# Performance work log

Measured on AMD Instinct MI355X. Metric: run time of the kernel, lower is better.

Reference implementation:

```python
import jax, jax.numpy as jnp
import numpy as np

D = 32          # embedding_size
B = 16384       # batch_size
P = 16          # neighbor_sample_size (paths per item per hop)
NE = 100000     # n_entity
NU = 100000     # n_user
NR = 32         # n_relation
N_ITER = 2


def setup_inputs() -> dict:
    key = jax.random.key(0)
    ks = jax.random.split(key, 20)
    s = 0.1
    nrm = lambda k, sh: jax.random.normal(k, sh, dtype=jnp.float32) * s
    inp = {
        "user_table": nrm(ks[0], (NU, D)),
        "ent_table": nrm(ks[1], (NE, D)),
        "rel_table": nrm(ks[2], (NR, D)),
        # PyTorch LSTM params, gate order (i, f, g, o)
        "w_ih0": nrm(ks[3], (4 * D, 2 * D)),
        "w_hh0": nrm(ks[4], (4 * D, D)),
        "b_ih0": nrm(ks[5], (4 * D,)),
        "b_hh0": nrm(ks[6], (4 * D,)),
        "w_ih1": nrm(ks[7], (4 * D, 2 * D)),
        "w_hh1": nrm(ks[8], (4 * D, D)),
        "b_ih1": nrm(ks[9], (4 * D,)),
        "b_hh1": nrm(ks[10], (4 * D,)),
        "agg_w": nrm(ks[11], (D, D)),
        "agg_b": nrm(ks[12], (D,)),
        "users": jax.random.randint(ks[13], (B,), 0, NU),
        "items": jax.random.randint(ks[14], (B,), 0, NE),
        "ratings": jax.random.randint(ks[15], (B,), 0, 2),
        # hop h path table: [n_entity, P, 2*(h+1)+1]; values < 32 valid for both tables
        "lp0": jax.random.randint(ks[16], (NE, P, 3), 0, 32),
        "lp1": jax.random.randint(ks[17], (NE, P, 5), 0, 32),
    }
    return inp


def _lstm_last(seq, w_ih, w_hh, b_ih, b_hh):
    # seq: [N, T, 2D] -> final hidden state [N, D], PyTorch gate order i,f,g,o
    N = seq.shape[0]
    H = w_hh.shape[1]
    bias = b_ih + b_hh

    def step(carry, x):
        h, c = carry
        g = x @ w_ih.T + h @ w_hh.T + bias
        i, f, gg, o = jnp.split(g, 4, axis=-1)
        c = jax.nn.sigmoid(f) * c + jax.nn.sigmoid(i) * jnp.tanh(gg)
        h = jax.nn.sigmoid(o) * jnp.tanh(c)
        return (h, c), None

    h0 = jnp.zeros((N, H), seq.dtype)
    (h, _), _ = jax.lax.scan(step, (h0, h0), jnp.swapaxes(seq, 0, 1))
    return h


def _forward(user_table, ent_table, rel_table, lstm_params, agg_w, agg_b,
             users, items, ratings, lps):
    u = user_table[users]                # [B, D]
    items_emb = ent_table[items]         # [B, D]
    for hop in range(N_ITER):
        lp = lps[hop]
        w_ih, w_hh, b_ih, b_hh = lstm_params[hop]
        il = lp[items]                   # [B, P, 2*(hop+1)+1]
        seed_e = ent_table[il[:, :, 0]]  # [B, P, D]
        u_b = jnp.broadcast_to(u[:, None, :], seed_e.shape)
        first = jnp.concatenate([u_b, seed_e], -1)[:, :, None, :]   # [B,P,1,2D]
        rel_e = rel_table[il[:, :, 1::2]]                            # [B,P,hop+1,D]
        tail_e = ent_table[il[:, :, 2::2]]                           # [B,P,hop+1,D]
        rest = jnp.concatenate([rel_e, tail_e], -1)                  # [B,P,hop+1,2D]
        seq = jnp.concatenate([first, rest], 2).reshape(B * P, hop + 2, 2 * D)
        h = _lstm_last(seq, w_ih, w_hh, b_ih, b_hh)                  # [B*P, D]
        final = h.reshape(B, P, D).sum(axis=1)                       # hidden_out sum
        items_emb = (items_emb + final) @ agg_w.T + agg_b            # 'sum' aggregator
    scores = jnp.sum(u * items_emb, axis=-1)                         # [B]
    r = ratings.astype(scores.dtype)
    # stable BCE on sigmoid(scores)
    loss = -jnp.mean(r * jax.nn.log_sigmoid(scores) + (1.0 - r) * jax.nn.log_sigmoid(-scores))
    return loss, jax.nn.sigmoid(scores)


def reference(user_table, ent_table, rel_table,
              w_ih0, w_hh0, b_ih0, b_hh0,
              w_ih1, w_hh1, b_ih1, b_hh1,
              agg_w, agg_b,
              users, items, ratings, lp0, lp1):
    lstm_params = [(w_ih0, w_hh0, b_ih0, b_hh0), (w_ih1, w_hh1, b_ih1, b_hh1)]
    loss, scores_normalized = _forward(user_table, ent_table, rel_table,
                                       lstm_params, agg_w, agg_b,
                                       users, items, ratings, (lp0, lp1))
    return (loss, scores_normalized, items)
```

## Files before the change

### kernel.cpp

```cpp
#include <hip/hip_runtime.h>
#include <math.h>

#define D  32
#define BN 16384
#define PP 16

typedef __bf16 bf16x8 __attribute__((ext_vector_type(8)));
typedef __bf16 bf16x4 __attribute__((ext_vector_type(4)));
typedef float  floatx4 __attribute__((ext_vector_type(4)));

#define K1 1.44269504088896341f
#define K2 2.88539008177792681f

#define TR_OFF    0
#define TE_OFF    8448
#define BIAS_OFF  16896
#define WU_OFF    17408
#define WHH_OFF   27648
#define IMG_BYTES 37888
#define LDS_BYTES (IMG_BYTES + 8 * 1280)

__device__ __forceinline__ float sigf(float x) {
    float e = __builtin_amdgcn_exp2f(-x * K1);
    return __builtin_amdgcn_rcpf(1.0f + e);
}
__device__ __forceinline__ float logsigf(float x) {
    float ax = fabsf(x);
    float l = log1pf(__expf(-ax));
    return (x >= 0.0f) ? -l : x - l;
}
__device__ __forceinline__ floatx4 cvt4(bf16x4 v) {
    floatx4 r = { (float)v[0], (float)v[1], (float)v[2], (float)v[3] };
    return r;
}
__device__ __forceinline__ bf16x8 loadu8(const float* __restrict__ p) {
    float4 a = ((const float4*)p)[0], b = ((const float4*)p)[1];
    bf16x8 r = { (__bf16)a.x, (__bf16)a.y, (__bf16)a.z, (__bf16)a.w,
                 (__bf16)b.x, (__bf16)b.y, (__bf16)b.z, (__bf16)b.w };
    return r;
}

__global__ __launch_bounds__(256)
void prep_tables(const float* __restrict__ ent, const float* __restrict__ rel,
                 const float* __restrict__ wih0, const float* __restrict__ whh0,
                 const float* __restrict__ bih0, const float* __restrict__ bhh0,
                 const float* __restrict__ wih1, const float* __restrict__ whh1,
                 const float* __restrict__ bih1, const float* __restrict__ bhh1,
                 float* __restrict__ imgs_f)
{
    const int id = blockIdx.x * 256 + threadIdx.x;
    if (id < 16384) {
        const int hop = id >> 13;
        const int rest = id & 8191;
        const int tab = rest >> 12;
        const int k   = (rest >> 7) & 31;
        const int g   = rest & 127;
        const float* wih = hop ? wih1 : wih0;
        char* base = (char*)imgs_f + (size_t)hop * IMG_BYTES;
        if (tab == 0) {
            const float* w = wih + (size_t)g * 64;
            const float* s = rel + (size_t)k * 32;
            float a = (hop ? bih1[g] + bhh1[g] : bih0[g] + bhh0[g]);
            #pragma unroll
            for (int d = 0; d < 32; ++d) a = fmaf(w[d], s[d], a);
            *((__bf16*)(base + TR_OFF) + k * 132 + g) = (__bf16)a;
        } else {
            const float* w = wih + (size_t)g * 64 + 32;
            const float* s = ent + (size_t)k * 32;
            float a = 0.0f;
            #pragma unroll
            for (int d = 0; d < 32; ++d) a = fmaf(w[d], s[d], a);
            *((__bf16*)(base + TE_OFF) + k * 132 + g) = (__bf16)a;
        }
    } else if (id < 32768) {
        const int id2 = id - 16384;
        const int hop = id2 >> 13;
        const int rest = id2 & 8191;
        const int mat  = rest >> 12;
        const int e    = rest & 4095;
        const int gate = e >> 5, d = e & 31;
        char* base = (char*)imgs_f + (size_t)hop * IMG_BYTES;
        float v;
        if (mat == 0) v = (hop ? wih1 : wih0)[(size_t)gate * 64 + d];
        else          v = (hop ? whh1 : whh0)[(size_t)gate * 32 + d];
        *((__bf16*)(base + (mat ? WHH_OFF : WU_OFF)) + gate * 40 + d) = (__bf16)v;
    } else if (id < 33024) {
        const int id3 = id - 32768;
        const int hop = id3 >> 7;
        const int g   = id3 & 127;
        char* base = (char*)imgs_f + (size_t)hop * IMG_BYTES;
        ((float*)(base + BIAS_OFF))[g] = hop ? (bih1[g] + bhh1[g])
                                             : (bih0[g] + bhh0[g]);
    }
}

template<bool FIRST, bool LAST>
__device__ __forceinline__ void nonlin(
    floatx4* __restrict__ acc, float* __restrict__ cst,
    float* __restrict__ hlo, float* __restrict__ hhi,
    char* __restrict__ Hw, int q, int bnl)
{
    #pragma unroll
    for (int hf = 0; hf < 2; ++hf) {
        float* hout = hf ? hhi : hlo;
        #pragma unroll
        for (int r = 0; r < 4; ++r) {
            float gi = acc[0 + hf][r], gf = acc[2 + hf][r],
                  gg = acc[4 + hf][r], go = acc[6 + hf][r];
            float Ai = 1.0f + __builtin_amdgcn_exp2f(-gi * K1);
            float Af = 1.0f + __builtin_amdgcn_exp2f(-gf * K1);
            float G2 = __builtin_amdgcn_exp2f(gg * K2);
            float Gp = G2 + 1.0f, Gm = G2 - 1.0f;
            float cold = FIRST ? 0.0f : cst[hf * 4 + r];
            float num = cold * Ai * Gp + Gm * Af;
            float c = num * __builtin_amdgcn_rcpf(Af * Ai * Gp);
            cst[hf * 4 + r] = c;
            float Ao = 1.0f + __builtin_amdgcn_exp2f(-go * K1);
            float C2 = __builtin_amdgcn_exp2f(c * K2);
            hout[r] = (C2 - 1.0f) * __builtin_amdgcn_rcpf(Ao * (C2 + 1.0f));
        }
    }
    if (!LAST) {
        bf16x4 plo = { (__bf16)hlo[0], (__bf16)hlo[1], (__bf16)hlo[2], (__bf16)hlo[3] };
        bf16x4 phi = { (__bf16)hhi[0], (__bf16)hhi[1], (__bf16)hhi[2], (__bf16)hhi[3] };
        *(bf16x4*)(Hw + bnl * 80 + 8 * q)      = plo;
        *(bf16x4*)(Hw + bnl * 80 + 32 + 8 * q) = phi;
    }
}

__global__ __launch_bounds__(256, 3)
void hop_mfma(const float* __restrict__ user_table,
              const int*   __restrict__ users,
              const int*   __restrict__ items,
              const int*   __restrict__ lp0,
              const int*   __restrict__ lp1,
              const float* __restrict__ imgs_f,
              float* __restrict__ F0,
              float* __restrict__ F1)
{
    __shared__ __align__(16) char lds[LDS_BYTES];

    const bool second = blockIdx.x & 1;
    const int  idx    = blockIdx.x >> 1;
    const int tid  = threadIdx.x;
    const int lane = tid & 63;
    const int wave = tid >> 6;
    const int q    = lane >> 4;
    const int bnl  = lane & 15;

    {
        const float4* g = (const float4*)((const char*)imgs_f +
                                          (second ? IMG_BYTES : 0));
        float4* l = (float4*)lds;
        #pragma unroll
        for (int i = 0; i < 10; ++i) {
            int k = i * 256 + tid;
            if (k < IMG_BYTES / 16) l[k] = g[k];
        }
    }

    const char* Tr  = lds + TR_OFF;
    const char* Te  = lds + TE_OFF;
    const char* Wu  = lds + WU_OFF;
    const char* Whh = lds + WHH_OFF;
    char* HwA = lds + IMG_BYTES + (wave * 2 + 0) * 1280;
    char* HwB = lds + IMG_BYTES + (wave * 2 + 1) * 1280;

    const int fbA = idx * 8 + wave;
    const int fbB = fbA + 4;
    const int L   = second ? 5 : 3;
    const int* lp = second ? lp1 : lp0;
    const int* __restrict__ ilA = lp + ((size_t)items[fbA] * PP + bnl) * L;
    const int* __restrict__ ilB = lp + ((size_t)items[fbB] * PP + bnl) * L;

    bf16x8 buA = loadu8(user_table + (size_t)users[fbA] * D + q * 8);
    bf16x8 buB = loadu8(user_table + (size_t)users[fbB] * D + q * 8);

    __syncthreads();

    float cstA[8], cstB[8], hloA[4], hhiA[4], hloB[4], hhiB[4];

    {
        const int sA = ilA[0], sB = ilB[0];
        floatx4 accA[8], accB[8];
        #pragma unroll
        for (int mt = 0; mt < 8; ++mt) {
            const int go = 16 * mt + 4 * q;
            floatx4 bv = *(const floatx4*)(lds + BIAS_OFF + go * 4);
            accA[mt] = bv + cvt4(*(const bf16x4*)(Te + sA * 264 + go * 2));
            accB[mt] = bv + cvt4(*(const bf16x4*)(Te + sB * 264 + go * 2));
        }
        #pragma unroll
        for (int mt = 0; mt < 8; ++mt) {
            bf16x8 wu = *(const bf16x8*)(Wu + (16 * mt + bnl) * 80 + q * 16);
            accA[mt] = __builtin_amdgcn_mfma_f32_16x16x32_bf16(wu, buA, accA[mt], 0, 0, 0);
            accB[mt] = __builtin_amdgcn_mfma_f32_16x16x32_bf16(wu, buB, accB[mt], 0, 0, 0);
        }
        nonlin<true, false>(accA, cstA, hloA, hhiA, HwA, q, bnl);
        nonlin<true, false>(accB, cstB, hloB, hhiB, HwB, q, bnl);
    }

    #pragma unroll
    for (int t = 1; t < 3; ++t) {
        if (t == 2 && !second) break;
        const bool last = (t == (second ? 2 : 1));
        const int jA = ilA[2 * t - 1], kA = ilA[2 * t];
        const int jB = ilB[2 * t - 1], kB = ilB[2 * t];
        floatx4 accA[8], accB[8];
        #pragma unroll
        for (int mt = 0; mt < 8; ++mt) {
            const int go = 16 * mt + 4 * q;
            accA[mt] = cvt4(*(const bf16x4*)(Tr + jA * 264 + go * 2))
                     + cvt4(*(const bf16x4*)(Te + kA * 264 + go * 2));
            accB[mt] = cvt4(*(const bf16x4*)(Tr + jB * 264 + go * 2))
                     + cvt4(*(const bf16x4*)(Te + kB * 264 + go * 2));
        }
        bf16x8 bhA = *(const bf16x8*)(HwA + bnl * 80 + q * 16);
        bf16x8 bhB = *(const bf16x8*)(HwB + bnl * 80 + q * 16);
        #pragma unroll
        for (int mt = 0; mt < 8; ++mt) {
            bf16x8 wh = *(const bf16x8*)(Whh + (16 * mt + bnl) * 80 + q * 16);
            accA[mt] = __builtin_amdgcn_mfma_f32_16x16x32_bf16(wh, bhA, accA[mt], 0, 0, 0);
            accB[mt] = __builtin_amdgcn_mfma_f32_16x16x32_bf16(wh, bhB, accB[mt], 0, 0, 0);
        }
        if (last) {
            nonlin<false, true>(accA, cstA, hloA, hhiA, HwA, q, bnl);
            nonlin<false, true>(accB, cstB, hloB, hhiB, HwB, q, bnl);
        } else {
            nonlin<false, false>(accA, cstA, hloA, hhiA, HwA, q, bnl);
            nonlin<false, false>(accB, cstB, hloB, hhiB, HwB, q, bnl);
        }
    }

    #pragma unroll
    for (int r = 0; r < 4; ++r) {
        #pragma unroll
        for (int m = 1; m < 16; m <<= 1) {
            hloA[r] += __shfl_xor(hloA[r], m);
            hhiA[r] += __shfl_xor(hhiA[r], m);
            hloB[r] += __shfl_xor(hloB[r], m);
            hhiB[r] += __shfl_xor(hhiB[r], m);
        }
    }
    if (bnl == 0) {
        float* Fout = (second ? F1 : F0);
        float4 vloA = { hloA[0], hloA[1], hloA[2], hloA[3] };
        float4 vhiA = { hhiA[0], hhiA[1], hhiA[2], hhiA[3] };
        float4 vloB = { hloB[0], hloB[1], hloB[2], hloB[3] };
        float4 vhiB = { hhiB[0], hhiB[1], hhiB[2], hhiB[3] };
        *(float4*)(Fout + (size_t)fbA * D + 4 * q)      = vloA;
        *(float4*)(Fout + (size_t)fbA * D + 16 + 4 * q) = vhiA;
        *(float4*)(Fout + (size_t)fbB * D + 4 * q)      = vloB;
        *(float4*)(Fout + (size_t)fbB * D + 16 + 4 * q) = vhiB;
    }
}

__global__ __launch_bounds__(256)
void chain_score(const float* __restrict__ user_table,
                 const float* __restrict__ ent_table,
                 const float* __restrict__ agg_w,
                 const float* __restrict__ agg_b,
                 const int*   __restrict__ users,
                 const int*   __restrict__ items,
                 const int*   __restrict__ ratings,
                 const float* __restrict__ F0,
                 const float* __restrict__ F1,
                 float* __restrict__ out,
                 float* __restrict__ partials)
{
    __shared__ float s[8][33];
    __shared__ float red[8];
    const int tid = threadIdx.x;
    const int bb  = tid >> 5;
    const int j   = tid & 31;
    const int b   = blockIdx.x * 8 + bb;
    const int it  = items[b];

    s[bb][j] = ent_table[(size_t)it * D + j] + F0[(size_t)b * D + j];
    __syncthreads();
    const float* __restrict__ w = agg_w + (size_t)j * D;
    float e0 = agg_b[j];
    #pragma unroll
    for (int k = 0; k < D; ++k) e0 = fmaf(s[bb][k], w[k], e0);
    __syncthreads();
    s[bb][j] = e0 + F1[(size_t)b * D + j];
    __syncthreads();
    float e1 = agg_b[j];
    #pragma unroll
    for (int k = 0; k < D; ++k) e1 = fmaf(s[bb][k], w[k], e1);

    float prod = user_table[(size_t)users[b] * D + j] * e1;
    #pragma unroll
    for (int m = 1; m < 32; m <<= 1) prod += __shfl_xor(prod, m);
    if (j == 0) {
        out[1 + b]      = sigf(prod);
        out[1 + BN + b] = (float)it;
        float r = (float)ratings[b];
        red[bb] = r * logsigf(prod) + (1.0f - r) * logsigf(-prod);
    }
    __syncthreads();
    if (tid == 0) {
        float t = 0.0f;
        #pragma unroll
        for (int qq = 0; qq < 8; ++qq) t += red[qq];
        partials[blockIdx.x] = t;
    }
}

__global__ __launch_bounds__(256)
void loss_kernel(const float* __restrict__ partials, float* __restrict__ out)
{
    __shared__ float red[4];
    const int t = threadIdx.x;
    float v = 0.0f;
    #pragma unroll
    for (int qq = 0; qq < 8; ++qq) v += partials[qq * 256 + t];
    #pragma unroll
    for (int m = 1; m < 64; m <<= 1) v += __shfl_xor(v, m);
    if ((t & 63) == 0) red[t >> 6] = v;
    __syncthreads();
    if (t == 0) out[0] = -(red[0] + red[1] + red[2] + red[3]) / (float)BN;
}

extern "C" void kernel_launch(void* const* d_in, const int* in_sizes, int n_in,
                              void* d_out, int out_size, void* d_ws, size_t ws_size,
                              hipStream_t stream)
{
    const float* user_table = (const float*)d_in[0];
    const float* ent_table  = (const float*)d_in[1];
    const float* rel_table  = (const float*)d_in[2];
    const float* w_ih0 = (const float*)d_in[3];
    const float* w_hh0 = (const float*)d_in[4];
    const float* b_ih0 = (const float*)d_in[5];
    const float* b_hh0 = (const float*)d_in[6];
    const float* w_ih1 = (const float*)d_in[7];
    const float* w_hh1 = (const float*)d_in[8];
    const float* b_ih1 = (const float*)d_in[9];
    const float* b_hh1 = (const float*)d_in[10];
    const float* agg_w = (const float*)d_in[11];
    const float* agg_b = (const float*)d_in[12];
    const int* users   = (const int*)d_in[13];
    const int* items   = (const int*)d_in[14];
    const int* ratings = (const int*)d_in[15];
    const int* lp0     = (const int*)d_in[16];
    const int* lp1     = (const int*)d_in[17];
    float* out = (float*)d_out;

    float* ws       = (float*)d_ws;
    float* F0       = ws;
    float* F1       = ws + (size_t)BN * D;
    float* partials = ws + 2 * (size_t)BN * D;
    float* imgs     = ws + 2 * (size_t)BN * D + 2048;

    prep_tables<<<130, 256, 0, stream>>>(ent_table, rel_table,
        w_ih0, w_hh0, b_ih0, b_hh0, w_ih1, w_hh1, b_ih1, b_hh1, imgs);
    hop_mfma<<<4096, 256, 0, stream>>>(
        user_table, users, items, lp0, lp1, imgs, F0, F1);
    chain_score<<<BN / 8, 256, 0, stream>>>(
        user_table, ent_table, agg_w, agg_b, users, items, ratings,
        F0, F1, out, partials);
    loss_kernel<<<1, 256, 0, stream>>>(partials, out);
}
```

Measured before the change: 233.8 us.

## Precompute full fp32 relation-entity gate table in global memory instead of LDS tables

Prep now builds a combined 32x32x128 fp32 table of input-projection gate values (relation+entity+bias) per hop in global memory, plus a bias-folded first-step table. The hop kernel reads gate preactivations directly with one float4 global load per tile instead of two bf16 LDS lookups plus conversion and add. LDS per block shrinks to the weight images and hidden buffers, reducing the per-block staging copy and allowing higher occupancy. In exchange, lookups go to a 1 MB L2-resident table with random access, and prep does more work (262k dot products). Path indices are also preloaded into registers.

New measurement: 270.2 us. +15.6%, slower.

```diff
diff --git a/kernel.cpp b/kernel.cpp
--- a/kernel.cpp
+++ b/kernel.cpp
@@ -12,13 +12,11 @@
 #define K1 1.44269504088896341f
 #define K2 2.88539008177792681f
 
-#define TR_OFF    0
-#define TE_OFF    8448
-#define BIAS_OFF  16896
-#define WU_OFF    17408
-#define WHH_OFF   27648
-#define IMG_BYTES 37888
-#define LDS_BYTES (IMG_BYTES + 8 * 1280)
+#define WU_OFF     0
+#define WHH_OFF    10240
+#define WIMG_BYTES 20480
+#define H_OFF      20480
+#define LDS_BYTES  (WIMG_BYTES + 8 * 1280)
 
 __device__ __forceinline__ float sigf(float x) {
     float e = __builtin_amdgcn_exp2f(-x * K1);
@@ -28,10 +26,6 @@
     float ax = fabsf(x);
     float l = log1pf(__expf(-ax));
     return (x >= 0.0f) ? -l : x - l;
-}
-__device__ __forceinline__ floatx4 cvt4(bf16x4 v) {
-    floatx4 r = { (float)v[0], (float)v[1], (float)v[2], (float)v[3] };
-    return r;
 }
 __device__ __forceinline__ bf16x8 loadu8(const float* __restrict__ p) {
     float4 a = ((const float4*)p)[0], b = ((const float4*)p)[1];
@@ -46,51 +40,61 @@
                  const float* __restrict__ bih0, const float* __restrict__ bhh0,
                  const float* __restrict__ wih1, const float* __restrict__ whh1,
                  const float* __restrict__ bih1, const float* __restrict__ bhh1,
-                 float* __restrict__ imgs_f)
+                 float* __restrict__ T0, float* __restrict__ T,
+                 float* __restrict__ wimg)
 {
     const int id = blockIdx.x * 256 + threadIdx.x;
     if (id < 16384) {
-        const int hop = id >> 13;
+        const int hop  = id >> 13;
         const int rest = id & 8191;
-        const int tab = rest >> 12;
-        const int k   = (rest >> 7) & 31;
-        const int g   = rest & 127;
-        const float* wih = hop ? wih1 : wih0;
-        char* base = (char*)imgs_f + (size_t)hop * IMG_BYTES;
-        if (tab == 0) {
-            const float* w = wih + (size_t)g * 64;
-            const float* s = rel + (size_t)k * 32;
-            float a = (hop ? bih1[g] + bhh1[g] : bih0[g] + bhh0[g]);
-            #pragma unroll
-            for (int d = 0; d < 32; ++d) a = fmaf(w[d], s[d], a);
-            *((__bf16*)(base + TR_OFF) + k * 132 + g) = (__bf16)a;
-        } else {
-            const float* w = wih + (size_t)g * 64 + 32;
-            const float* s = ent + (size_t)k * 32;
-            float a = 0.0f;
-            #pragma unroll
-            for (int d = 0; d < 32; ++d) a = fmaf(w[d], s[d], a);
-            *((__bf16*)(base + TE_OFF) + k * 132 + g) = (__bf16)a;
-        }
-    } else if (id < 32768) {
-        const int id2 = id - 16384;
-        const int hop = id2 >> 13;
-        const int rest = id2 & 8191;
         const int mat  = rest >> 12;
         const int e    = rest & 4095;
         const int gate = e >> 5, d = e & 31;
-        char* base = (char*)imgs_f + (size_t)hop * IMG_BYTES;
-        float v;
-        if (mat == 0) v = (hop ? wih1 : wih0)[(size_t)gate * 64 + d];
-        else          v = (hop ? whh1 : whh0)[(size_t)gate * 32 + d];
-        *((__bf16*)(base + (mat ? WHH_OFF : WU_OFF)) + gate * 40 + d) = (__bf16)v;
-    } else if (id < 33024) {
-        const int id3 = id - 32768;
-        const int hop = id3 >> 7;
-        const int g   = id3 & 127;
-        char* base = (char*)imgs_f + (size_t)hop * IMG_BYTES;
-        ((float*)(base + BIAS_OFF))[g] = hop ? (bih1[g] + bhh1[g])
-                                             : (bih0[g] + bhh0[g]);
+        float v = mat ? (hop ? whh1 : whh0)[(size_t)gate * 32 + d]
+                      : (hop ? wih1 : wih0)[(size_t)gate * 64 + d];
+        __bf16* base = (__bf16*)((char*)wimg + hop * WIMG_BYTES + mat * 10240);
+        base[gate * 40 + d] = (__bf16)v;
+    } else if (id < 16384 + 262144) {
+        const int idt = id - 16384;
+        const int hop = idt >> 17;
+        const int r   = idt & 131071;
+        const int j   = r >> 12;
+        const int k   = (r >> 7) & 31;
+        const int g   = r & 127;
+        const float* wih = hop ? wih1 : wih0;
+        const float4* w4 = (const float4*)(wih + (size_t)g * 64);
+        const float4* r4 = (const float4*)(rel + (size_t)j * 32);
+        const float4* e4 = (const float4*)(ent + (size_t)k * 32);
+        float a = hop ? bih1[g] + bhh1[g] : bih0[g] + bhh0[g];
+        #pragma unroll
+        for (int i = 0; i < 8; ++i) {
+            float4 w = w4[i], x = r4[i];
+            a = fmaf(w.x, x.x, a); a = fmaf(w.y, x.y, a);
+            a = fmaf(w.z, x.z, a); a = fmaf(w.w, x.w, a);
+        }
+        #pragma unroll
+        for (int i = 0; i < 8; ++i) {
+            float4 w = w4[8 + i], x = e4[i];
+            a = fmaf(w.x, x.x, a); a = fmaf(w.y, x.y, a);
+            a = fmaf(w.z, x.z, a); a = fmaf(w.w, x.w, a);
+        }
+        T[(size_t)hop * 131072 + r] = a;
+    } else if (id < 16384 + 262144 + 8192) {
+        const int idb = id - 16384 - 262144;
+        const int hop = idb >> 12;
+        const int k   = (idb >> 7) & 31;
+        const int g   = idb & 127;
+        const float* wih = hop ? wih1 : wih0;
+        const float4* w4 = (const float4*)(wih + (size_t)g * 64);
+        const float4* e4 = (const float4*)(ent + (size_t)k * 32);
+        float a = hop ? bih1[g] + bhh1[g] : bih0[g] + bhh0[g];
+        #pragma unroll
+        for (int i = 0; i < 8; ++i) {
+            float4 w = w4[8 + i], x = e4[i];
+            a = fmaf(w.x, x.x, a); a = fmaf(w.y, x.y, a);
+            a = fmaf(w.z, x.z, a); a = fmaf(w.w, x.w, a);
+        }
+        T0[(size_t)hop * 4096 + k * 128 + g] = a;
     }
 }
 
@@ -134,7 +138,9 @@
               const int*   __restrict__ items,
               const int*   __restrict__ lp0,
               const int*   __restrict__ lp1,
-              const float* __restrict__ imgs_f,
+              const float* __restrict__ wimg,
+              const float* __restrict__ T0g,
+              const float* __restrict__ Tg,
               float* __restrict__ F0,
               float* __restrict__ F1)
 {
@@ -149,22 +155,17 @@
     const int bnl  = lane & 15;
 
     {
-        const float4* g = (const float4*)((const char*)imgs_f +
-                                          (second ? IMG_BYTES : 0));
-        float4* l = (float4*)lds;
-        #pragma unroll
-        for (int i = 0; i < 10; ++i) {
-            int k = i * 256 + tid;
-            if (k < IMG_BYTES / 16) l[k] = g[k];
-        }
-    }
-
-    const char* Tr  = lds + TR_OFF;
-    const char* Te  = lds + TE_OFF;
+        const float4* g4 = (const float4*)((const char*)wimg +
+                                           (second ? WIMG_BYTES : 0));
+        float4* l4 = (float4*)lds;
+        #pragma unroll
+        for (int i = 0; i < 5; ++i) l4[i * 256 + tid] = g4[i * 256 + tid];
+    }
+
     const char* Wu  = lds + WU_OFF;
     const char* Whh = lds + WHH_OFF;
-    char* HwA = lds + IMG_BYTES + (wave * 2 + 0) * 1280;
-    char* HwB = lds + IMG_BYTES + (wave * 2 + 1) * 1280;
+    char* HwA = lds + H_OFF + (wave * 2 + 0) * 1280;
+    char* HwB = lds + H_OFF + (wave * 2 + 1) * 1280;
 
     const int fbA = idx * 8 + wave;
     const int fbB = fbA + 4;
@@ -172,23 +173,31 @@
     const int* lp = second ? lp1 : lp0;
     const int* __restrict__ ilA = lp + ((size_t)items[fbA] * PP + bnl) * L;
     const int* __restrict__ ilB = lp + ((size_t)items[fbB] * PP + bnl) * L;
+    int sqA[5], sqB[5];
+    #pragma unroll
+    for (int i = 0; i < 5; ++i) {
+        sqA[i] = (i < L) ? ilA[i] : 0;
+        sqB[i] = (i < L) ? ilB[i] : 0;
+    }
 
     bf16x8 buA = loadu8(user_table + (size_t)users[fbA] * D + q * 8);
     bf16x8 buB = loadu8(user_table + (size_t)users[fbB] * D + q * 8);
 
+    const float* T0h = T0g + (second ? 4096 : 0);
+    const float* Th  = Tg  + (second ? 131072 : 0);
+
     __syncthreads();
 
     float cstA[8], cstB[8], hloA[4], hhiA[4], hloB[4], hhiB[4];
 
     {
-        const int sA = ilA[0], sB = ilB[0];
+        const float* tA = T0h + sqA[0] * 128 + 4 * q;
+        const float* tB = T0h + sqB[0] * 128 + 4 * q;
         floatx4 accA[8], accB[8];
         #pragma unroll
         for (int mt = 0; mt < 8; ++mt) {
-            const int go = 16 * mt + 4 * q;
-            floatx4 bv = *(const floatx4*)(lds + BIAS_OFF + go * 4);
-            accA[mt] = bv + cvt4(*(const bf16x4*)(Te + sA * 264 + go * 2));
-            accB[mt] = bv + cvt4(*(const bf16x4*)(Te + sB * 264 + go * 2));
+            accA[mt] = *(const floatx4*)(tA + 16 * mt);
+            accB[mt] = *(const floatx4*)(tB + 16 * mt);
         }
         #pragma unroll
         for (int mt = 0; mt < 8; ++mt) {
@@ -204,16 +213,13 @@
     for (int t = 1; t < 3; ++t) {
         if (t == 2 && !second) break;
         const bool last = (t == (second ? 2 : 1));
-        const int jA = ilA[2 * t - 1], kA = ilA[2 * t];
-        const int jB = ilB[2 * t - 1], kB = ilB[2 * t];
+        const float* tA = Th + (((sqA[2 * t - 1]) << 5) + sqA[2 * t]) * 128 + 4 * q;
+        const float* tB = Th + (((sqB[2 * t - 1]) << 5) + sqB[2 * t]) * 128 + 4 * q;
         floatx4 accA[8], accB[8];
         #pragma unroll
         for (int mt = 0; mt < 8; ++mt) {
-            const int go = 16 * mt + 4 * q;
-            accA[mt] = cvt4(*(const bf16x4*)(Tr + jA * 264 + go * 2))
-                     + cvt4(*(const bf16x4*)(Te + kA * 264 + go * 2));
-            accB[mt] = cvt4(*(const bf16x4*)(Tr + jB * 264 + go * 2))
-                     + cvt4(*(const bf16x4*)(Te + kB * 264 + go * 2));
+            accA[mt] = *(const floatx4*)(tA + 16 * mt);
+            accB[mt] = *(const floatx4*)(tB + 16 * mt);
         }
         bf16x8 bhA = *(const bf16x8*)(HwA + bnl * 80 + q * 16);
         bf16x8 bhB = *(const bf16x8*)(HwB + bnl * 80 + q * 16);
@@ -348,14 +354,16 @@
 
     float* ws       = (float*)d_ws;
     float* F0       = ws;
-    float* F1       = ws + (size_t)BN * D;
-    float* partials = ws + 2 * (size_t)BN * D;
-    float* imgs     = ws + 2 * (size_t)BN * D + 2048;
-
-    prep_tables<<<130, 256, 0, stream>>>(ent_table, rel_table,
-        w_ih0, w_hh0, b_ih0, b_hh0, w_ih1, w_hh1, b_ih1, b_hh1, imgs);
+    float* F1       = F0 + (size_t)BN * D;
+    float* partials = F1 + (size_t)BN * D;
+    float* T0       = partials + 2048;
+    float* T        = T0 + 8192;
+    float* wimg     = T + 262144;
+
+    prep_tables<<<1120, 256, 0, stream>>>(ent_table, rel_table,
+        w_ih0, w_hh0, b_ih0, b_hh0, w_ih1, w_hh1, b_ih1, b_hh1, T0, T, wimg);
     hop_mfma<<<4096, 256, 0, stream>>>(
-        user_table, users, items, lp0, lp1, imgs, F0, F1);
+        user_table, users, items, lp0, lp1, wimg, T0, T, F0, F1);
     chain_score<<<BN / 8, 256, 0, stream>>>(
         user_table, ent_table, agg_w, agg_b, users, items, ratings,
         F0, F1, out, partials);
```
